# Kernel optimization log

Measured on AMD Instinct MI355X. Metric: run time of the kernel, lower is better.

The kernel has to match this reference:

```python
import jax, jax.numpy as jnp
import numpy as np

B, NQ, NKV = 4, 2048, 2048
D_MODEL, N_HEADS, D_K = 1024, 16, 64


def setup_inputs() -> dict:
    key = jax.random.key(0)
    ks = jax.random.split(key, 7)
    s = 1.0 / np.sqrt(D_MODEL)
    return {
        "x": jax.random.normal(ks[0], (B, NQ, D_MODEL), jnp.float32),
        "encoding": jax.random.normal(ks[1], (B, NKV, D_MODEL), jnp.float32),
        "position_bias": jax.random.normal(ks[2], (1, N_HEADS, NQ, NKV), jnp.float32),
        "Wq": jax.random.normal(ks[3], (D_MODEL, D_MODEL), jnp.float32) * s,
        "Wk": jax.random.normal(ks[4], (D_MODEL, D_MODEL), jnp.float32) * s,
        "Wv": jax.random.normal(ks[5], (D_MODEL, D_MODEL), jnp.float32) * s,
        "Wo": jax.random.normal(ks[6], (D_MODEL, D_MODEL), jnp.float32) * s,
    }


def _split_heads(t):
    b, n, _ = t.shape
    return t.reshape(b, n, N_HEADS, D_K).transpose(0, 2, 1, 3)


def reference(x, encoding, position_bias, Wq, Wk, Wv, Wo):
    # Projections (flax Dense, no bias): y = x @ kernel
    Q = _split_heads(x @ Wq)            # [B,H,NQ,Dk]
    K = _split_heads(encoding @ Wk)     # [B,H,NKV,Dk]
    V = _split_heads(encoding @ Wv)     # [B,H,NKV,Dk]
    # T5-style: NO 1/sqrt(d_k) scaling; additive position bias before softmax
    scores = jnp.einsum('bhqd,bhkd->bhqk', Q, K) + position_bias
    attn = jax.nn.softmax(scores, axis=-1)
    ctx = jnp.einsum('bhqk,bhkd->bhqd', attn, V)    # [B,H,NQ,Dk]
    ctx = ctx.transpose(0, 2, 1, 3).reshape(x.shape[0], x.shape[1], D_MODEL)
    return ctx @ Wo
```

## Files before the change

kernel.cpp:

```cpp
#include <hip/hip_runtime.h>

#define B_   4
#define NQ_  2048
#define NKV_ 2048
#define H_   16
#define DK_  64
#define DM_  1024
#define DKV_ 2048

typedef _Float16 f16x8 __attribute__((ext_vector_type(8)));
typedef _Float16 f16x4 __attribute__((ext_vector_type(4)));
typedef float    f32x4 __attribute__((ext_vector_type(4)));

__device__ __forceinline__ void gload_lds16(const void* g, void* l) {
  __builtin_amdgcn_global_load_lds(
      (const __attribute__((address_space(1))) unsigned int*)g,
      (__attribute__((address_space(3))) unsigned int*)l, 16, 0, 0);
}

__global__ __launch_bounds__(256) void cast_f16(const float* __restrict__ in,
                                                _Float16* __restrict__ out, int n4) {
  int i = blockIdx.x * 256 + threadIdx.x;
  if (i >= n4) return;
  float4 v = ((const float4*)in)[i];
  f16x4 o = {(_Float16)v.x, (_Float16)v.y, (_Float16)v.z, (_Float16)v.w};
  *(f16x4*)(out + (size_t)i * 4) = o;
}

__global__ __launch_bounds__(256) void wtrans(const float* __restrict__ W,
                                              _Float16* __restrict__ Wt) {
  __shared__ float tile[32][33];
  int bx = blockIdx.x & 31, by = blockIdx.x >> 5;
  int tx = threadIdx.x & 31, ty = threadIdx.x >> 5;
#pragma unroll
  for (int j = 0; j < 4; ++j)
    tile[ty + j * 8][tx] = W[(size_t)(by * 32 + ty + j * 8) * 1024 + bx * 32 + tx];
  __syncthreads();
#pragma unroll
  for (int j = 0; j < 4; ++j)
    Wt[(size_t)(bx * 32 + ty + j * 8) * 1024 + by * 32 + tx] = (_Float16)tile[tx][ty + j * 8];
}

template <int F32OUT>
__global__ __launch_bounds__(256, 2) void gemm_bt(const _Float16* __restrict__ A,
                                                  const _Float16* __restrict__ Bt,
                                                  void* __restrict__ Cp,
                                                  int M, int N, int K) {
  __shared__ _Float16 As[128 * 32];
  __shared__ _Float16 Bs[128 * 32];
  const int nbn = N >> 7;
  const int bm = blockIdx.x / nbn, bn = blockIdx.x % nbn;
  const int t = threadIdx.x, w = t >> 6, l = t & 63;
  const int lr = l & 15, lg = l >> 4;
  const int wr = w >> 1, wc = w & 1;
  const int m0 = bm << 7, n0 = bn << 7;

  f32x4 acc[4][4] = {};

  for (int k0 = 0; k0 < K; k0 += 32) {
#pragma unroll
    for (int p = 0; p < 2; ++p) {
      int off = p * 4096 + w * 1024 + l * 16;
      int row = off >> 6;
      int col = (off & 63) >> 1;
      gload_lds16(A  + (size_t)(m0 + row) * K + k0 + col, (char*)As + p * 4096 + w * 1024);
      gload_lds16(Bt + (size_t)(n0 + row) * K + k0 + col, (char*)Bs + p * 4096 + w * 1024);
    }
    __syncthreads();
    f16x8 af[4], bq[4];
#pragma unroll
    for (int i = 0; i < 4; ++i) {
      af[i] = *(const f16x8*)((const char*)As + (wr * 64 + i * 16 + lr) * 64 + lg * 16);
      bq[i] = *(const f16x8*)((const char*)Bs + (wc * 64 + i * 16 + lr) * 64 + lg * 16);
    }
#pragma unroll
    for (int i = 0; i < 4; ++i)
#pragma unroll
      for (int j = 0; j < 4; ++j)
        acc[i][j] = __builtin_amdgcn_mfma_f32_16x16x32_f16(af[i], bq[j], acc[i][j], 0, 0, 0);
    __syncthreads();
  }
#pragma unroll
  for (int i = 0; i < 4; ++i)
#pragma unroll
    for (int j = 0; j < 4; ++j)
#pragma unroll
      for (int r = 0; r < 4; ++r) {
        size_t row = m0 + wr * 64 + i * 16 + lg * 4 + r;
        size_t col = n0 + wc * 64 + j * 16 + lr;
        if (F32OUT) ((float*)Cp)[row * N + col] = acc[i][j][r];
        else ((_Float16*)Cp)[row * N + col] = (_Float16)acc[i][j][r];
      }
}

__global__ __launch_bounds__(256) void vtrans(const _Float16* __restrict__ KVb,
                                              _Float16* __restrict__ Vt) {
  __shared__ _Float16 tile[64][72];
  int idx = blockIdx.x;
  int kt = idx & 31, h = (idx >> 5) & 15, b = idx >> 9;
  int kv0 = kt << 6;
  int t = threadIdx.x;
#pragma unroll
  for (int p = 0; p < 2; ++p) {
    int c = t + p * 256;
    int row = c >> 3, cb = (c & 7) * 16;
    f16x8 v = *(const f16x8*)(KVb + (size_t)(b * NKV_ + kv0 + row) * DKV_ + 1024 + h * 64 + cb / 2);
    *(f16x8*)((char*)&tile[row][0] + cb) = v;
  }
  __syncthreads();
  int d = t & 63, j0 = (t >> 6) * 2;
#pragma unroll
  for (int jj = 0; jj < 2; ++jj) {
    int kvs = (j0 + jj) * 8;
    f16x8 o;
#pragma unroll
    for (int u = 0; u < 8; ++u) o[u] = tile[kvs + u][d];
    *(f16x8*)(Vt + ((size_t)((b * H_ + h) * 64 + d)) * NKV_ + kv0 + kvs) = o;
  }
}

__global__ __launch_bounds__(256, 2) void attn(const _Float16* __restrict__ Qb,
                                               const _Float16* __restrict__ KVb,
                                               const _Float16* __restrict__ Vt,
                                               const float* __restrict__ bias,
                                               _Float16* __restrict__ ctx) {
  __shared__ _Float16 Ks[64 * 64];
  __shared__ _Float16 Vs[64 * 64];
  __shared__ _Float16 Ps[4][16 * 64];
  const float LOG2E = 1.44269504f;
  int idx = blockIdx.x;
  int b = idx & 3, qt = (idx >> 2) & 31, h = idx >> 7;
  int t = threadIdx.x, w = t >> 6, l = t & 63, lr = l & 15, lg = l >> 4;
  int qw = (qt << 6) + (w << 4);

  const _Float16* qp = Qb + (size_t)(b * NQ_ + qw + lr) * DM_ + h * 64 + lg * 8;
  f16x8 aq0 = *(const f16x8*)qp;
  f16x8 aq1 = *(const f16x8*)(qp + 32);
#pragma unroll
  for (int u = 0; u < 8; ++u) { aq0[u] = aq0[u] * (_Float16)LOG2E; aq1[u] = aq1[u] * (_Float16)LOG2E; }

  f32x4 acc[4] = {};
  float mrow[4] = {-1e30f, -1e30f, -1e30f, -1e30f};
  float lsum[4] = {0.f, 0.f, 0.f, 0.f};

  const _Float16* Kbase = KVb + (size_t)b * NKV_ * DKV_ + h * 64;
  const _Float16* Vtb   = Vt + (size_t)(b * H_ + h) * 64 * NKV_;
  const float*    biasb = bias + ((size_t)h * NQ_ + qw + lg * 4) * NKV_;

  const int srow = t >> 3;
  const int scb  = (t & 7) * 16;

  f16x8 kreg[2], vreg[2];
  float bv[4][4], bvn[4][4];

  auto LOADKV = [&](int kv0) {
#pragma unroll
    for (int p = 0; p < 2; ++p) {
      int row = srow + p * 32;
      kreg[p] = *(const f16x8*)(Kbase + (size_t)(kv0 + row) * DKV_ + scb / 2);
      vreg[p] = *(const f16x8*)(Vtb + (size_t)row * NKV_ + kv0 + scb / 2);
    }
  };
  auto LOADBIAS = [&](int kv0, float (&dst)[4][4]) {
#pragma unroll
    for (int r = 0; r < 4; ++r) {
      const float* bp = biasb + (size_t)r * NKV_ + kv0 + lr;
#pragma unroll
      for (int nt = 0; nt < 4; ++nt) dst[nt][r] = bp[nt * 16] * LOG2E;
    }
  };

  LOADKV(0);
  LOADBIAS(0, bv);

  for (int it = 0; it < 32; ++it) {
    const int kv0 = it << 6;

#pragma unroll
    for (int p = 0; p < 2; ++p) {
      int row = srow + p * 32;
      int off = (row * 128 + scb) ^ ((row & 7) << 4);
      *(f16x8*)((char*)Ks + off) = kreg[p];
      *(f16x8*)((char*)Vs + off) = vreg[p];
    }
    __syncthreads();

    const int kvn = (it < 31) ? kv0 + 64 : kv0;
    LOADKV(kvn);

    f32x4 s[4];
    __builtin_amdgcn_s_setprio(1);
#pragma unroll
    for (int nt = 0; nt < 4; ++nt) {
      int row = nt * 16 + lr;
      int sw = (row & 7) << 4;
      f16x8 kf0 = *(const f16x8*)((char*)Ks + ((row * 128 + lg * 16) ^ sw));
      f16x8 kf1 = *(const f16x8*)((char*)Ks + ((row * 128 + 64 + lg * 16) ^ sw));
      f32x4 z = {0.f, 0.f, 0.f, 0.f};
      z = __builtin_amdgcn_mfma_f32_16x16x32_f16(aq0, kf0, z, 0, 0, 0);
      s[nt] = __builtin_amdgcn_mfma_f32_16x16x32_f16(aq1, kf1, z, 0, 0, 0);
    }
    __builtin_amdgcn_s_setprio(0);

#pragma unroll
    for (int nt = 0; nt < 4; ++nt)
#pragma unroll
      for (int r = 0; r < 4; ++r) s[nt][r] += bv[nt][r];
    LOADBIAS((it < 31) ? kv0 + 64 : kv0, bvn);

#pragma unroll
    for (int r = 0; r < 4; ++r) {
      float v = fmaxf(fmaxf(s[0][r], s[1][r]), fmaxf(s[2][r], s[3][r]));
      v = fmaxf(v, __shfl_xor(v, 1));
      v = fmaxf(v, __shfl_xor(v, 2));
      v = fmaxf(v, __shfl_xor(v, 4));
      v = fmaxf(v, __shfl_xor(v, 8));
      float mn = fmaxf(mrow[r], v);
      float corr = exp2f(mrow[r] - mn);
      mrow[r] = mn;
      float rs = 0.f;
#pragma unroll
      for (int nt = 0; nt < 4; ++nt) {
        float p = exp2f(s[nt][r] - mn);
        s[nt][r] = p;
        rs += p;
      }
      rs += __shfl_xor(rs, 1);
      rs += __shfl_xor(rs, 2);
      rs += __shfl_xor(rs, 4);
      rs += __shfl_xor(rs, 8);
      lsum[r] = lsum[r] * corr + rs;
#pragma unroll
      for (int nt = 0; nt < 4; ++nt) acc[nt][r] *= corr;
    }

#pragma unroll
    for (int r = 0; r < 4; ++r) {
      int row = lg * 4 + r;
      int sw = (row & 7) << 4;
#pragma unroll
      for (int nt = 0; nt < 4; ++nt)
        *(_Float16*)((char*)Ps[w] + ((row * 128 + (nt * 16 + lr) * 2) ^ sw)) =
            (_Float16)s[nt][r];
    }

    __builtin_amdgcn_s_setprio(1);
#pragma unroll
    for (int kk = 0; kk < 2; ++kk) {
      f16x8 pa = *(const f16x8*)((char*)Ps[w] +
                 ((lr * 128 + kk * 64 + lg * 16) ^ ((lr & 7) << 4)));
#pragma unroll
      for (int nt = 0; nt < 4; ++nt) {
        int row = nt * 16 + lr;
        f16x8 vf = *(const f16x8*)((char*)Vs +
                 ((row * 128 + kk * 64 + lg * 16) ^ ((row & 7) << 4)));
        acc[nt] = __builtin_amdgcn_mfma_f32_16x16x32_f16(pa, vf, acc[nt], 0, 0, 0);
      }
    }
    __builtin_amdgcn_s_setprio(0);
    __syncthreads();

#pragma unroll
    for (int nt = 0; nt < 4; ++nt)
#pragma unroll
      for (int r = 0; r < 4; ++r) bv[nt][r] = bvn[nt][r];
  }

#pragma unroll
  for (int r = 0; r < 4; ++r) {
    float inv = 1.0f / lsum[r];
#pragma unroll
    for (int nt = 0; nt < 4; ++nt) {
      float o = acc[nt][r] * inv;
      size_t q = qw + lg * 4 + r;
      ctx[((size_t)b * NQ_ + q) * DM_ + h * 64 + nt * 16 + lr] = (_Float16)o;
    }
  }
}

extern "C" void kernel_launch(void* const* d_in, const int* in_sizes, int n_in,
                              void* d_out, int out_size, void* d_ws, size_t ws_size,
                              hipStream_t stream) {
  const float* x    = (const float*)d_in[0];
  const float* enc  = (const float*)d_in[1];
  const float* bias = (const float*)d_in[2];
  const float* Wq   = (const float*)d_in[3];
  const float* Wk   = (const float*)d_in[4];
  const float* Wv   = (const float*)d_in[5];
  const float* Wo   = (const float*)d_in[6];
  char* ws = (char*)d_ws;
  const size_t MiB = 1024 * 1024;
  _Float16* WqT   = (_Float16*)(ws + 0 * MiB);
  _Float16* WkT   = (_Float16*)(ws + 2 * MiB);
  _Float16* WvT   = (_Float16*)(ws + 4 * MiB);
  _Float16* WoT   = (_Float16*)(ws + 6 * MiB);
  _Float16* xf    = (_Float16*)(ws + 8 * MiB);
  _Float16* encf  = (_Float16*)(ws + 24 * MiB);
  _Float16* Qb    = (_Float16*)(ws + 40 * MiB);
  _Float16* KVb   = (_Float16*)(ws + 56 * MiB);
  _Float16* Vt    = (_Float16*)(ws + 88 * MiB);
  _Float16* ctxf  = (_Float16*)(ws + 104 * MiB);

  wtrans<<<1024, 256, 0, stream>>>(Wq, WqT);
  wtrans<<<1024, 256, 0, stream>>>(Wk, WkT);
  wtrans<<<1024, 256, 0, stream>>>(Wv, WvT);
  wtrans<<<1024, 256, 0, stream>>>(Wo, WoT);
  cast_f16<<<8192, 256, 0, stream>>>(x, xf, 2097152);
  cast_f16<<<8192, 256, 0, stream>>>(enc, encf, 2097152);
  gemm_bt<0><<<512, 256, 0, stream>>>(xf, WqT, Qb, 8192, 1024, 1024);
  gemm_bt<0><<<1024, 256, 0, stream>>>(encf, WkT, KVb, 8192, 2048, 1024);
  vtrans<<<2048, 256, 0, stream>>>(KVb, Vt);
  attn<<<2048, 256, 0, stream>>>(Qb, KVb, Vt, bias, ctxf);
  gemm_bt<1><<<512, 256, 0, stream>>>(ctxf, WoT, d_out, 8192, 1024, 1024);
}
```

Baseline: 398.1 us.

## Transpose attention MFMAs so each lane owns one query row, with lazy rescaling

Swaps the MFMA operand order so the score and output tiles are transposed and each lane holds a single query row. The row max and sum then need only two cross-lane shuffles instead of four per row, and the bias and ctx accesses become float4 and f16x4 vector accesses. The bias is now loaded inside the loop with no register prefetch, and the softmax rescale is skipped unless the max grows by more than 8 (lazy rescaling). It also raises launch bounds to 4 waves per SIMD, which may cost register spills and exposes bias load latency in exchange for fewer VGPRs.

```diff
diff --git a/kernel.cpp b/kernel.cpp
--- a/kernel.cpp
+++ b/kernel.cpp
@@ -119,7 +119,7 @@
   }
 }
 
-__global__ __launch_bounds__(256, 2) void attn(const _Float16* __restrict__ Qb,
+__global__ __launch_bounds__(256, 4) void attn(const _Float16* __restrict__ Qb,
                                                const _Float16* __restrict__ KVb,
                                                const _Float16* __restrict__ Vt,
                                                const float* __restrict__ bias,
@@ -140,18 +140,17 @@
   for (int u = 0; u < 8; ++u) { aq0[u] = aq0[u] * (_Float16)LOG2E; aq1[u] = aq1[u] * (_Float16)LOG2E; }
 
   f32x4 acc[4] = {};
-  float mrow[4] = {-1e30f, -1e30f, -1e30f, -1e30f};
-  float lsum[4] = {0.f, 0.f, 0.f, 0.f};
+  float mrow = -1e30f;
+  float lsum = 0.f;
 
   const _Float16* Kbase = KVb + (size_t)b * NKV_ * DKV_ + h * 64;
   const _Float16* Vtb   = Vt + (size_t)(b * H_ + h) * 64 * NKV_;
-  const float*    biasb = bias + ((size_t)h * NQ_ + qw + lg * 4) * NKV_;
+  const float*    biasq = bias + ((size_t)h * NQ_ + qw + lr) * NKV_ + lg * 4;
 
   const int srow = t >> 3;
   const int scb  = (t & 7) * 16;
 
   f16x8 kreg[2], vreg[2];
-  float bv[4][4], bvn[4][4];
 
   auto LOADKV = [&](int kv0) {
 #pragma unroll
@@ -161,17 +160,8 @@
       vreg[p] = *(const f16x8*)(Vtb + (size_t)row * NKV_ + kv0 + scb / 2);
     }
   };
-  auto LOADBIAS = [&](int kv0, float (&dst)[4][4]) {
-#pragma unroll
-    for (int r = 0; r < 4; ++r) {
-      const float* bp = biasb + (size_t)r * NKV_ + kv0 + lr;
-#pragma unroll
-      for (int nt = 0; nt < 4; ++nt) dst[nt][r] = bp[nt * 16] * LOG2E;
-    }
-  };
 
   LOADKV(0);
-  LOADBIAS(0, bv);
 
   for (int it = 0; it < 32; ++it) {
     const int kv0 = it << 6;
@@ -187,6 +177,11 @@
 
     const int kvn = (it < 31) ? kv0 + 64 : kv0;
     LOADKV(kvn);
+
+    float4 bv4[4];
+#pragma unroll
+    for (int nt = 0; nt < 4; ++nt)
+      bv4[nt] = *(const float4*)(biasq + kv0 + nt * 16);
 
     f32x4 s[4];
     __builtin_amdgcn_s_setprio(1);
@@ -197,84 +192,81 @@
       f16x8 kf0 = *(const f16x8*)((char*)Ks + ((row * 128 + lg * 16) ^ sw));
       f16x8 kf1 = *(const f16x8*)((char*)Ks + ((row * 128 + 64 + lg * 16) ^ sw));
       f32x4 z = {0.f, 0.f, 0.f, 0.f};
-      z = __builtin_amdgcn_mfma_f32_16x16x32_f16(aq0, kf0, z, 0, 0, 0);
-      s[nt] = __builtin_amdgcn_mfma_f32_16x16x32_f16(aq1, kf1, z, 0, 0, 0);
+      z = __builtin_amdgcn_mfma_f32_16x16x32_f16(kf0, aq0, z, 0, 0, 0);
+      s[nt] = __builtin_amdgcn_mfma_f32_16x16x32_f16(kf1, aq1, z, 0, 0, 0);
     }
     __builtin_amdgcn_s_setprio(0);
 
 #pragma unroll
+    for (int nt = 0; nt < 4; ++nt) {
+      s[nt][0] = fmaf(bv4[nt].x, LOG2E, s[nt][0]);
+      s[nt][1] = fmaf(bv4[nt].y, LOG2E, s[nt][1]);
+      s[nt][2] = fmaf(bv4[nt].z, LOG2E, s[nt][2]);
+      s[nt][3] = fmaf(bv4[nt].w, LOG2E, s[nt][3]);
+    }
+
+    float pmax = fmaxf(fmaxf(s[0][0], s[0][1]), fmaxf(s[0][2], s[0][3]));
+#pragma unroll
+    for (int nt = 1; nt < 4; ++nt)
+      pmax = fmaxf(pmax, fmaxf(fmaxf(s[nt][0], s[nt][1]), fmaxf(s[nt][2], s[nt][3])));
+    pmax = fmaxf(pmax, __shfl_xor(pmax, 16));
+    pmax = fmaxf(pmax, __shfl_xor(pmax, 32));
+
+    if (__any(pmax > mrow + 8.0f)) {
+      float mn = fmaxf(mrow, pmax);
+      float corr = exp2f(mrow - mn);
+      mrow = mn;
+      lsum *= corr;
+#pragma unroll
+      for (int nt = 0; nt < 4; ++nt)
+#pragma unroll
+        for (int r = 0; r < 4; ++r) acc[nt][r] *= corr;
+    }
+
+    float rs = 0.f;
+#pragma unroll
     for (int nt = 0; nt < 4; ++nt)
 #pragma unroll
-      for (int r = 0; r < 4; ++r) s[nt][r] += bv[nt][r];
-    LOADBIAS((it < 31) ? kv0 + 64 : kv0, bvn);
-
-#pragma unroll
-    for (int r = 0; r < 4; ++r) {
-      float v = fmaxf(fmaxf(s[0][r], s[1][r]), fmaxf(s[2][r], s[3][r]));
-      v = fmaxf(v, __shfl_xor(v, 1));
-      v = fmaxf(v, __shfl_xor(v, 2));
-      v = fmaxf(v, __shfl_xor(v, 4));
-      v = fmaxf(v, __shfl_xor(v, 8));
-      float mn = fmaxf(mrow[r], v);
-      float corr = exp2f(mrow[r] - mn);
-      mrow[r] = mn;
-      float rs = 0.f;
-#pragma unroll
-      for (int nt = 0; nt < 4; ++nt) {
-        float p = exp2f(s[nt][r] - mn);
+      for (int r = 0; r < 4; ++r) {
+        float p = exp2f(s[nt][r] - mrow);
         s[nt][r] = p;
         rs += p;
       }
-      rs += __shfl_xor(rs, 1);
-      rs += __shfl_xor(rs, 2);
-      rs += __shfl_xor(rs, 4);
-      rs += __shfl_xor(rs, 8);
-      lsum[r] = lsum[r] * corr + rs;
-#pragma unroll
-      for (int nt = 0; nt < 4; ++nt) acc[nt][r] *= corr;
-    }
-
-#pragma unroll
-    for (int r = 0; r < 4; ++r) {
-      int row = lg * 4 + r;
-      int sw = (row & 7) << 4;
-#pragma unroll
-      for (int nt = 0; nt < 4; ++nt)
-        *(_Float16*)((char*)Ps[w] + ((row * 128 + (nt * 16 + lr) * 2) ^ sw)) =
-            (_Float16)s[nt][r];
+    rs += __shfl_xor(rs, 16);
+    rs += __shfl_xor(rs, 32);
+    lsum += rs;
+
+#pragma unroll
+    for (int nt = 0; nt < 4; ++nt) {
+      f16x4 pk = {(_Float16)s[nt][0], (_Float16)s[nt][1],
+                  (_Float16)s[nt][2], (_Float16)s[nt][3]};
+      int off = (lr * 128 + nt * 32 + lg * 8) ^ ((lr & 7) << 4);
+      *(f16x4*)((char*)Ps[w] + off) = pk;
     }
 
     __builtin_amdgcn_s_setprio(1);
 #pragma unroll
     for (int kk = 0; kk < 2; ++kk) {
-      f16x8 pa = *(const f16x8*)((char*)Ps[w] +
+      f16x8 pb = *(const f16x8*)((char*)Ps[w] +
                  ((lr * 128 + kk * 64 + lg * 16) ^ ((lr & 7) << 4)));
 #pragma unroll
       for (int nt = 0; nt < 4; ++nt) {
         int row = nt * 16 + lr;
         f16x8 vf = *(const f16x8*)((char*)Vs +
                  ((row * 128 + kk * 64 + lg * 16) ^ ((row & 7) << 4)));
-        acc[nt] = __builtin_amdgcn_mfma_f32_16x16x32_f16(pa, vf, acc[nt], 0, 0, 0);
+        acc[nt] = __builtin_amdgcn_mfma_f32_16x16x32_f16(vf, pb, acc[nt], 0, 0, 0);
       }
     }
     __builtin_amdgcn_s_setprio(0);
     __syncthreads();
-
-#pragma unroll
-    for (int nt = 0; nt < 4; ++nt)
-#pragma unroll
-      for (int r = 0; r < 4; ++r) bv[nt][r] = bvn[nt][r];
-  }
-
-#pragma unroll
-  for (int r = 0; r < 4; ++r) {
-    float inv = 1.0f / lsum[r];
-#pragma unroll
-    for (int nt = 0; nt < 4; ++nt) {
-      float o = acc[nt][r] * inv;
-      size_t q = qw + lg * 4 + r;
-      ctx[((size_t)b * NQ_ + q) * DM_ + h * 64 + nt * 16 + lr] = (_Float16)o;
-    }
+  }
+
+  float inv = 1.0f / lsum;
+#pragma unroll
+  for (int nt = 0; nt < 4; ++nt) {
+    f16x4 o = {(_Float16)(acc[nt][0] * inv), (_Float16)(acc[nt][1] * inv),
+               (_Float16)(acc[nt][2] * inv), (_Float16)(acc[nt][3] * inv)};
+    *(f16x4*)(ctx + ((size_t)b * NQ_ + qw + lr) * DM_ + h * 64 + nt * 16 + lg * 4) = o;
   }
 }
 
```

After: 353.1 us. 1.13x faster.
